# Performance work log

Hardware: AMD Instinct MI355X
Metric: run time of the kernel (lower is better)

## Reference

```python
import jax, jax.numpy as jnp
import numpy as np

B, C_IN, C_OUT, N, L = 4, 128, 256, 4096, 4
D = C_OUT // 4
EPS_BN = 1e-5


def setup_inputs() -> dict:
    key = jax.random.key(0)
    ks = jax.random.split(key, 16)
    s_in = 1.0 / np.sqrt(C_IN)
    s_out = 1.0 / np.sqrt(C_OUT)
    return {
        "features": jax.random.normal(ks[0], (B, C_IN, N), dtype=jnp.float32),
        # LBR: conv1x1 -> BN -> ReLU -> conv1x1 -> BN -> ReLU
        "lbr_w1": jax.random.uniform(ks[1], (C_OUT, C_IN), jnp.float32, -s_in, s_in),
        "lbr_g1": jnp.ones((C_OUT,), jnp.float32),
        "lbr_b1": jnp.zeros((C_OUT,), jnp.float32),
        "lbr_w2": jax.random.uniform(ks[2], (C_OUT, C_OUT), jnp.float32, -s_out, s_out),
        "lbr_g2": jnp.ones((C_OUT,), jnp.float32),
        "lbr_b2": jnp.zeros((C_OUT,), jnp.float32),
        # per-layer OffsetAttention params (stacked on leading L axis)
        # q_conv and k_conv share the same weight (q_conv.weight = k_conv.weight)
        "attn_qk_w": jax.random.uniform(ks[3], (L, D, C_OUT), jnp.float32, -s_out, s_out),
        "attn_v_w": jax.random.uniform(ks[4], (L, C_OUT, C_OUT), jnp.float32, -s_out, s_out),
        "attn_v_b": jax.random.uniform(ks[5], (L, C_OUT), jnp.float32, -s_out, s_out),
        "attn_t_w": jax.random.uniform(ks[6], (L, C_OUT, C_OUT), jnp.float32, -s_out, s_out),
        "attn_t_b": jax.random.uniform(ks[7], (L, C_OUT), jnp.float32, -s_out, s_out),
        "attn_bn_g": jnp.ones((L, C_OUT), jnp.float32),
        "attn_bn_b": jnp.zeros((L, C_OUT), jnp.float32),
    }


def batchnorm1d(x, gamma, beta):
    # x: [B, C, N]; training-mode BN: batch stats over (B, N), biased variance
    mean = jnp.mean(x, axis=(0, 2), keepdims=True)
    var = jnp.mean(jnp.square(x - mean), axis=(0, 2), keepdims=True)
    xn = (x - mean) * jax.lax.rsqrt(var + EPS_BN)
    return xn * gamma[None, :, None] + beta[None, :, None]


def offset_attention(x, qk_w, v_w, v_b, t_w, t_b, bn_g, bn_b):
    # x: [B, C, N]
    K = jnp.einsum("dc,bcn->bdn", qk_w, x)            # [B, D, N]
    # Q = same conv, permuted to [B, N, D]; attention_map = Q @ K -> [B, N, N]
    attn = jnp.einsum("bdn,bdm->bnm", K, K)
    attn = jax.nn.softmax(attn, axis=-1)
    # extra L1 renorm over dim=1 (column-wise)
    attn = attn / (1e-9 + jnp.sum(attn, axis=1, keepdims=True))
    V = jnp.einsum("dc,bcn->bdn", v_w, x) + v_b[None, :, None]  # [B, C, N]
    new_feat = jnp.einsum("bcn,bnm->bcm", V, attn)    # [B, C, N]
    off = x - new_feat
    t = jnp.einsum("dc,bcn->bdn", t_w, off) + t_b[None, :, None]
    return jax.nn.relu(batchnorm1d(t, bn_g, bn_b))


def reference(features, lbr_w1, lbr_g1, lbr_b1, lbr_w2, lbr_g2, lbr_b2,
              attn_qk_w, attn_v_w, attn_v_b, attn_t_w, attn_t_b,
              attn_bn_g, attn_bn_b):
    # LBR stem
    h = jnp.einsum("dc,bcn->bdn", lbr_w1, features)
    h = jax.nn.relu(batchnorm1d(h, lbr_g1, lbr_b1))
    h = jnp.einsum("dc,bcn->bdn", lbr_w2, h)
    h = jax.nn.relu(batchnorm1d(h, lbr_g2, lbr_b2))
    # stacked offset attention; output concatenates attention outputs only
    outs = []
    cur = h
    for i in range(L):
        cur = offset_attention(cur, attn_qk_w[i], attn_v_w[i], attn_v_b[i],
                               attn_t_w[i], attn_t_b[i], attn_bn_g[i], attn_bn_b[i])
        outs.append(cur)
    return jnp.concatenate(outs, axis=1)  # [B, C_OUT*L, N]
```

## Files before the change

### kernel.cpp

```cpp
#include <hip/hip_runtime.h>
#include <hip/hip_bf16.h>
#include <math.h>

#define NPTS 4096
#define CO   256
#define CI   128
#define BB   4
#define DQ   64
#define LL   4
#define PST  136

typedef __attribute__((ext_vector_type(8))) short bf16x8;
typedef __attribute__((ext_vector_type(4))) float f32x4;

#define MFMA16(a,b,c) __builtin_amdgcn_mfma_f32_16x16x32_bf16((a),(b),(c),0,0,0)

__device__ __forceinline__ short fb(float x) {
  __hip_bfloat16 h = __float2bfloat16(x);
  return __builtin_bit_cast(short, h);
}
__device__ __forceinline__ float bf(short s) {
  unsigned u = ((unsigned)(unsigned short)s) << 16;
  return __builtin_bit_cast(float, u);
}

__global__ __launch_bounds__(256) void cvtw_k(
    const float* __restrict__ S, short* __restrict__ D, int n8)
{
  const int i = blockIdx.x * 256 + threadIdx.x;
  if (i < n8) {
    const float4 a = ((const float4*)S)[i * 2];
    const float4 b = ((const float4*)S)[i * 2 + 1];
    bf16x8 r;
    r[0] = fb(a.x); r[1] = fb(a.y); r[2] = fb(a.z); r[3] = fb(a.w);
    r[4] = fb(b.x); r[5] = fb(b.y); r[6] = fb(b.z); r[7] = fb(b.w);
    ((bf16x8*)D)[i] = r;
  }
}

__global__ __launch_bounds__(256) void tcvt_k(
    const float* __restrict__ X, long xbs, int C, short* __restrict__ XT)
{
  const int n0 = blockIdx.x * 64, c0 = blockIdx.y * 64, b = blockIdx.z;
  const int t = threadIdx.x, tl = t & 63, tg = t >> 6;
  __shared__ float xs[64][65];
#pragma unroll
  for (int r = 0; r < 16; ++r) {
    const int cc = tg * 16 + r;
    xs[cc][tl] = X[(long)b * xbs + (long)(c0 + cc) * NPTS + n0 + tl];
  }
  __syncthreads();
#pragma unroll
  for (int r = 0; r < 16; ++r) {
    const int nn = tg * 16 + r;
    XT[((long)b * NPTS + n0 + nn) * C + c0 + tl] = fb(xs[tl][nn]);
  }
}

template<int OMODE, bool BIAS>
__global__ __launch_bounds__(256) void conv_a(
    const short* __restrict__ XT, int C,
    const short* __restrict__ Wb, const float* __restrict__ bias,
    void* __restrict__ Yv, long ybs)
{
  const int n0 = blockIdx.x * 128, d0 = blockIdx.y * 64, b = blockIdx.z;
  const int tid = threadIdx.x, w = tid >> 6, l = tid & 63, lg = l >> 4, lr = l & 15;
  const short* xb = XT + (long)b * NPTS * C;
  f32x4 acc[8];
#pragma unroll
  for (int i = 0; i < 8; ++i) acc[i] = (f32x4){0.f, 0.f, 0.f, 0.f};
  const int dr = d0 + w * 16 + lr;
  for (int kc = 0; kc < C; kc += 32) {
    const bf16x8 af = *(const bf16x8*)&Wb[(long)dr * C + kc + lg * 8];
#pragma unroll
    for (int ni = 0; ni < 8; ++ni) {
      const bf16x8 bx = *(const bf16x8*)&xb[(long)(n0 + ni * 16 + lr) * C + kc + lg * 8];
      acc[ni] = MFMA16(af, bx, acc[ni]);
    }
  }
  float bv[4] = {0.f, 0.f, 0.f, 0.f};
  if (BIAS) {
    const float4 b4 = *(const float4*)&bias[d0 + w * 16 + lg * 4];
    bv[0] = b4.x; bv[1] = b4.y; bv[2] = b4.z; bv[3] = b4.w;
  }
  const int db = d0 + w * 16 + lg * 4;
#pragma unroll
  for (int ni = 0; ni < 8; ++ni) {
    const int n = n0 + ni * 16 + lr;
#pragma unroll
    for (int j = 0; j < 4; ++j) {
      const float o = acc[ni][j] + bv[j];
      if constexpr (OMODE == 0) {
        ((float*)Yv)[(long)b * ybs + (long)(db + j) * NPTS + n] = o;
      } else {
        ((short*)Yv)[(long)b * ybs + ((long)(n0 >> 7) * CO + db + j) * 128 + (n & 127)] = fb(o);
      }
    }
  }
}

__global__ __launch_bounds__(256) void conv_b(
    const short* __restrict__ XT, const short* __restrict__ Wb,
    short* __restrict__ KTo)
{
  const int n0 = blockIdx.x * 64, b = blockIdx.y;
  const int tid = threadIdx.x, w = tid >> 6, l = tid & 63, lg = l >> 4, lr = l & 15;
  const short* xb = XT + (long)b * NPTS * CO;
  f32x4 acc[4];
#pragma unroll
  for (int i = 0; i < 4; ++i) acc[i] = (f32x4){0.f, 0.f, 0.f, 0.f};
  const long nr = n0 + w * 16 + lr;
  for (int kc = 0; kc < CO; kc += 32) {
    const bf16x8 af = *(const bf16x8*)&xb[nr * CO + kc + lg * 8];
#pragma unroll
    for (int di = 0; di < 4; ++di) {
      const bf16x8 wf = *(const bf16x8*)&Wb[(long)(di * 16 + lr) * CO + kc + lg * 8];
      acc[di] = MFMA16(af, wf, acc[di]);
    }
  }
  short* Ko = KTo + (long)b * NPTS * DQ;
  const int nb = n0 + w * 16 + lg * 4;
#pragma unroll
  for (int j = 0; j < 4; ++j) {
#pragma unroll
    for (int di = 0; di < 4; ++di)
      Ko[(long)(nb + j) * DQ + di * 16 + lr] = fb(acc[di][j]);
  }
}

__global__ __launch_bounds__(256) void bnstats_k(
    const float* __restrict__ X, long xbs,
    float* __restrict__ mean, float* __restrict__ rstd)
{
  const int c = blockIdx.x, t = threadIdx.x;
  float s = 0.f, s2 = 0.f;
  for (int b = 0; b < BB; ++b) {
    const float4* p = (const float4*)(X + (long)b * xbs + (long)c * NPTS);
    for (int n = t; n < NPTS / 4; n += 256) {
      const float4 v = p[n];
      s  += v.x + v.y + v.z + v.w;
      s2 += v.x * v.x + v.y * v.y + v.z * v.z + v.w * v.w;
    }
  }
#pragma unroll
  for (int o = 32; o > 0; o >>= 1) { s += __shfl_down(s, o); s2 += __shfl_down(s2, o); }
  __shared__ float a1[4], a2[4];
  if ((t & 63) == 0) { a1[t >> 6] = s; a2[t >> 6] = s2; }
  __syncthreads();
  if (t == 0) {
    const float S  = a1[0] + a1[1] + a1[2] + a1[3];
    const float S2 = a2[0] + a2[1] + a2[2] + a2[3];
    const float m  = S / (float)(BB * NPTS);
    const float v  = S2 / (float)(BB * NPTS) - m * m;
    mean[c] = m;
    rstd[c] = rsqrtf(v + 1e-5f);
  }
}

template<bool WF32, bool WBF>
__global__ __launch_bounds__(256) void bnrelu_t(
    const float* __restrict__ X, long xbs,
    const float* __restrict__ mean, const float* __restrict__ rstd,
    const float* __restrict__ g, const float* __restrict__ be,
    float* __restrict__ Yf, long ybs, short* __restrict__ XT)
{
  const int n0 = blockIdx.x * 64, c0 = blockIdx.y * 64, b = blockIdx.z;
  const int t = threadIdx.x, tl = t & 63, tg = t >> 6;
  __shared__ float xs[64][65];
#pragma unroll
  for (int r = 0; r < 16; ++r) {
    const int cc = tg * 16 + r, c = c0 + cc;
    float v = X[(long)b * xbs + (long)c * NPTS + n0 + tl];
    v = fmaxf((v - mean[c]) * rstd[c] * g[c] + be[c], 0.f);
    if (WF32) Yf[(long)b * ybs + (long)c * NPTS + n0 + tl] = v;
    xs[cc][tl] = v;
  }
  __syncthreads();
  if (WBF) {
#pragma unroll
    for (int r = 0; r < 16; ++r) {
      const int nn = tg * 16 + r;
      XT[((long)b * NPTS + n0 + nn) * CO + c0 + tl] = fb(xs[tl][nn]);
    }
  }
}

__global__ __launch_bounds__(256) void rowstats_mfma(
    const short* __restrict__ KT, float* __restrict__ pmax, float* __restrict__ psum)
{
  const int bid = blockIdx.x;
  const int b = (bid >> 1) & 3;
  const int idx = (bid >> 3) * 2 + (bid & 1);
  const int n0 = (idx & 63) * 64;
  const int chunk = idx >> 6;
  const int tid = threadIdx.x, w = tid >> 6, l = tid & 63, lg = l >> 4, lr = l & 15;
  const short* Kb = KT + (long)b * NPTS * DQ;
  const int nr = n0 + w * 16 + lr;
  const bf16x8 a0 = *(const bf16x8*)&Kb[(long)nr * DQ + lg * 8];
  const bf16x8 a1 = *(const bf16x8*)&Kb[(long)nr * DQ + 32 + lg * 8];

  float mx[4][4], sm[4][4];
#pragma unroll
  for (int p = 0; p < 4; ++p)
#pragma unroll
    for (int j = 0; j < 4; ++j) { mx[p][j] = -INFINITY; sm[p][j] = 0.f; }

  const int mc = chunk * (NPTS / 4);
  for (int m0 = mc; m0 < mc + NPTS / 4; m0 += 64) {
#pragma unroll
    for (int p = 0; p < 4; ++p) {
      const bf16x8 b0 = *(const bf16x8*)&Kb[(long)(m0 + p * 16 + lr) * DQ + lg * 8];
      const bf16x8 b1 = *(const bf16x8*)&Kb[(long)(m0 + p * 16 + lr) * DQ + 32 + lg * 8];
      f32x4 s = {0.f, 0.f, 0.f, 0.f};
      s = MFMA16(a0, b0, s);
      s = MFMA16(a1, b1, s);
#pragma unroll
      for (int j = 0; j < 4; ++j) {
        const float d = s[j] - mx[p][j];
        const float e = __expf(-fabsf(d));
        const bool gt = d > 0.f;
        sm[p][j] = gt ? fmaf(sm[p][j], e, 1.f) : (sm[p][j] + e);
        mx[p][j] = gt ? s[j] : mx[p][j];
      }
    }
  }
#pragma unroll
  for (int p = 1; p < 4; ++p)
#pragma unroll
    for (int j = 0; j < 4; ++j) {
      const float m2 = fmaxf(mx[0][j], mx[p][j]);
      sm[0][j] = sm[0][j] * __expf(mx[0][j] - m2) + sm[p][j] * __expf(mx[p][j] - m2);
      mx[0][j] = m2;
    }

  float mx0 = mx[0][0], mx1 = mx[0][1], mx2 = mx[0][2], mx3 = mx[0][3];
  float sm0 = sm[0][0], sm1 = sm[0][1], sm2 = sm[0][2], sm3 = sm[0][3];
#define MRG(MX, SM, OFF) { const float om_ = __shfl_xor(MX, OFF); \
  const float os_ = __shfl_xor(SM, OFF); \
  const float m2_ = fmaxf(MX, om_); \
  SM = SM * __expf(MX - m2_) + os_ * __expf(om_ - m2_); MX = m2_; }
#pragma unroll
  for (int off = 1; off < 16; off <<= 1) {
    MRG(mx0, sm0, off); MRG(mx1, sm1, off);
    MRG(mx2, sm2, off); MRG(mx3, sm3, off);
  }
  if (lr == 0) {
    const long base = ((long)chunk * BB + b) * NPTS + n0 + w * 16 + lg * 4;
    pmax[base + 0] = mx0; pmax[base + 1] = mx1; pmax[base + 2] = mx2; pmax[base + 3] = mx3;
    psum[base + 0] = sm0; psum[base + 1] = sm1; psum[base + 2] = sm2; psum[base + 3] = sm3;
  }
}

__global__ __launch_bounds__(256) void combine_k(
    const float* __restrict__ pmax, const float* __restrict__ psum,
    float* __restrict__ rmax, float* __restrict__ rinv)
{
  const long i = (long)blockIdx.x * 256 + threadIdx.x;
  const long st = (long)BB * NPTS;
  float m = pmax[i];
  m = fmaxf(m, pmax[st + i]); m = fmaxf(m, pmax[2 * st + i]); m = fmaxf(m, pmax[3 * st + i]);
  const float s = psum[i] * __expf(pmax[i] - m)
                + psum[st + i] * __expf(pmax[st + i] - m)
                + psum[2 * st + i] * __expf(pmax[2 * st + i] - m)
                + psum[3 * st + i] * __expf(pmax[3 * st + i] - m);
  rmax[i] = m;
  rinv[i] = 1.f / s;
}

__global__ __launch_bounds__(512) void pass2_mfma(
    const short* __restrict__ KT, const short* __restrict__ Vblk,
    const float* __restrict__ rmax, const float* __restrict__ rinv,
    short* __restrict__ XO)
{
  const int bid = blockIdx.x;
  const int b  = (bid >> 1) & 3;
  const int m0 = ((bid >> 3) * 2 + (bid & 1)) * 64;
  const int tid = threadIdx.x;
  const int w = tid >> 6, l = tid & 63, lg = l >> 4, lr = l & 15;
  const int NT = NPTS / 128;

  const short* Kb = KT + (long)b * NPTS * DQ;
  const short* Vb = Vblk + (long)b * CO * NPTS;
  const float* rmb = rmax + (long)b * NPTS;
  const float* rib = rinv + (long)b * NPTS;

  __shared__ short Ps[2][64][PST];
  __shared__ float cspart[8][64];
  __shared__ float csum[64];

  bf16x8 bK[4][2];
#pragma unroll
  for (int ms = 0; ms < 4; ++ms) {
    bK[ms][0] = *(const bf16x8*)&Kb[(long)(m0 + ms * 16 + lr) * DQ + lg * 8];
    bK[ms][1] = *(const bf16x8*)&Kb[(long)(m0 + ms * 16 + lr) * DQ + 32 + lg * 8];
  }

  f32x4 acc[4][2];
#pragma unroll
  for (int i = 0; i < 4; ++i) {
    acc[i][0] = (f32x4){0.f, 0.f, 0.f, 0.f};
    acc[i][1] = (f32x4){0.f, 0.f, 0.f, 0.f};
  }
  float cs[4] = {0.f, 0.f, 0.f, 0.f};
  const int c0 = w * 32;
  const int nb = w * 16;

  bf16x8 a0, a1;
  float4 rm4, ri4;

  auto sblk = [&](int dbuf) {
    f32x4 s[4];
#pragma unroll
    for (int ms = 0; ms < 4; ++ms) {
      s[ms] = (f32x4){0.f, 0.f, 0.f, 0.f};
      s[ms] = MFMA16(a0, bK[ms][0], s[ms]);
      s[ms] = MFMA16(a1, bK[ms][1], s[ms]);
    }
#pragma unroll
    for (int ms = 0; ms < 4; ++ms) {
      const float p0 = __expf(s[ms][0] - rm4.x) * ri4.x;
      const float p1 = __expf(s[ms][1] - rm4.y) * ri4.y;
      const float p2 = __expf(s[ms][2] - rm4.z) * ri4.z;
      const float p3 = __expf(s[ms][3] - rm4.w) * ri4.w;
      cs[ms] += p0 + p1 + p2 + p3;
      const unsigned u0 = ((unsigned)(unsigned short)fb(p1) << 16) | (unsigned short)fb(p0);
      const unsigned u1 = ((unsigned)(unsigned short)fb(p3) << 16) | (unsigned short)fb(p2);
      *(uint2*)&Ps[dbuf][ms * 16 + lr][nb + lg * 4] = make_uint2(u0, u1);
    }
  };

  a0  = *(const bf16x8*)&Kb[(long)(nb + lr) * DQ + lg * 8];
  a1  = *(const bf16x8*)&Kb[(long)(nb + lr) * DQ + 32 + lg * 8];
  rm4 = *(const float4*)&rmb[nb + lg * 4];
  ri4 = *(const float4*)&rib[nb + lg * 4];
  sblk(0);
  a0  = *(const bf16x8*)&Kb[(long)(128 + nb + lr) * DQ + lg * 8];
  a1  = *(const bf16x8*)&Kb[(long)(128 + nb + lr) * DQ + 32 + lg * 8];
  rm4 = *(const float4*)&rmb[128 + nb + lg * 4];
  ri4 = *(const float4*)&rib[128 + nb + lg * 4];

  for (int i = 0; i < NT; ++i) {
    const int n0 = i * 128;
    asm volatile("s_waitcnt lgkmcnt(0)" ::: "memory");
    __builtin_amdgcn_s_barrier();

    const short* vt = Vb + (long)(n0 >> 7) * CO * 128;
    bf16x8 vf[4][2];
#pragma unroll
    for (int kc = 0; kc < 4; ++kc) {
      vf[kc][0] = *(const bf16x8*)&vt[(long)(c0 + lr) * 128 + kc * 32 + lg * 8];
      vf[kc][1] = *(const bf16x8*)&vt[(long)(c0 + 16 + lr) * 128 + kc * 32 + lg * 8];
    }
    bf16x8 pa[4][4];
#pragma unroll
    for (int kc = 0; kc < 4; ++kc)
#pragma unroll
      for (int ms = 0; ms < 4; ++ms)
        pa[ms][kc] = *(const bf16x8*)&Ps[i & 1][ms * 16 + lr][kc * 32 + lg * 8];

    if (i + 1 < NT) {
      sblk((i + 1) & 1);
      if (i + 2 < NT) {
        a0  = *(const bf16x8*)&Kb[(long)((i + 2) * 128 + nb + lr) * DQ + lg * 8];
        a1  = *(const bf16x8*)&Kb[(long)((i + 2) * 128 + nb + lr) * DQ + 32 + lg * 8];
        rm4 = *(const float4*)&rmb[(i + 2) * 128 + nb + lg * 4];
        ri4 = *(const float4*)&rib[(i + 2) * 128 + nb + lg * 4];
      }
    }

#pragma unroll
    for (int kc = 0; kc < 4; ++kc)
#pragma unroll
      for (int ms = 0; ms < 4; ++ms) {
        acc[ms][0] = MFMA16(pa[ms][kc], vf[kc][0], acc[ms][0]);
        acc[ms][1] = MFMA16(pa[ms][kc], vf[kc][1], acc[ms][1]);
      }
  }

  __syncthreads();
#pragma unroll
  for (int ms = 0; ms < 4; ++ms) {
    float csv = cs[ms];
    csv += __shfl_xor(csv, 16); csv += __shfl_xor(csv, 32);
    if (lg == 0) cspart[w][ms * 16 + lr] = csv;
  }
  __syncthreads();
  if (tid < 64) {
    float s = 0.f;
#pragma unroll
    for (int ww = 0; ww < 8; ++ww) s += cspart[ww][tid];
    csum[tid] = s;
  }
  __syncthreads();

  short* XOb = XO + (long)b * NPTS * CO;
#pragma unroll
  for (int ms = 0; ms < 4; ++ms) {
#pragma unroll
    for (int j = 0; j < 4; ++j) {
      const int m = m0 + ms * 16 + lg * 4 + j;
      const float inv = 1.f / (1e-9f + csum[ms * 16 + lg * 4 + j]);
      const long i0 = (long)m * CO + c0 + lr;
      const long i1 = (long)m * CO + c0 + 16 + lr;
      XOb[i0] = fb(bf(XOb[i0]) - acc[ms][0][j] * inv);
      XOb[i1] = fb(bf(XOb[i1]) - acc[ms][1][j] * inv);
    }
  }
}

extern "C" void kernel_launch(void* const* d_in, const int* in_sizes, int n_in,
                              void* d_out, int out_size, void* d_ws, size_t ws_size,
                              hipStream_t stream)
{
  const float* feat = (const float*)d_in[0];
  const float* w1   = (const float*)d_in[1];
  const float* g1   = (const float*)d_in[2];
  const float* b1   = (const float*)d_in[3];
  const float* w2   = (const float*)d_in[4];
  const float* g2   = (const float*)d_in[5];
  const float* b2   = (const float*)d_in[6];
  const float* qkw  = (const float*)d_in[7];
  const float* vw   = (const float*)d_in[8];
  const float* vb   = (const float*)d_in[9];
  const float* tw   = (const float*)d_in[10];
  const float* tb   = (const float*)d_in[11];
  const float* bng  = (const float*)d_in[12];
  const float* bnb  = (const float*)d_in[13];

  float* out = (float*)d_out;

  short* xt    = (short*)d_ws;
  short* KTb   = xt + (long)BB * NPTS * CO;
  short* Vblk  = KTb + (long)BB * NPTS * DQ;
  short* wb1   = Vblk + (long)BB * CO * NPTS;
  short* wb2   = wb1 + (long)CO * CI;
  short* wqk   = wb2 + (long)CO * CO;
  short* wv    = wqk + (long)LL * DQ * CO;
  short* wt    = wv + (long)LL * CO * CO;
  float* pmaxb = (float*)(wt + (long)LL * CO * CO);
  float* psumb = pmaxb + (long)4 * BB * NPTS;
  float* rmaxb = psumb + (long)4 * BB * NPTS;
  float* rinvb = rmaxb + (long)BB * NPTS;
  float* meanb = rinvb + (long)BB * NPTS;
  float* rstdb = meanb + CO;

  const long OBS = (long)LL * CO * NPTS;
  float* h1 = out + (long)2 * CO * NPTS;
  float* x0 = out + (long)1 * CO * NPTS;

  const dim3 blk(256);

  cvtw_k<<<dim3((CO * CI / 8 + 255) / 256), blk, 0, stream>>>(w1, wb1, CO * CI / 8);
  cvtw_k<<<dim3((CO * CO / 8 + 255) / 256), blk, 0, stream>>>(w2, wb2, CO * CO / 8);
  cvtw_k<<<dim3((LL * DQ * CO / 8 + 255) / 256), blk, 0, stream>>>(qkw, wqk, LL * DQ * CO / 8);
  cvtw_k<<<dim3((LL * CO * CO / 8 + 255) / 256), blk, 0, stream>>>(vw, wv, LL * CO * CO / 8);
  cvtw_k<<<dim3((LL * CO * CO / 8 + 255) / 256), blk, 0, stream>>>(tw, wt, LL * CO * CO / 8);

  tcvt_k<<<dim3(64, 2, BB), blk, 0, stream>>>(feat, (long)CI * NPTS, CI, xt);
  conv_a<0, false><<<dim3(32, 4, BB), blk, 0, stream>>>(xt, CI, wb1, nullptr, h1, OBS);
  bnstats_k<<<dim3(CO), blk, 0, stream>>>(h1, OBS, meanb, rstdb);
  bnrelu_t<false, true><<<dim3(64, 4, BB), blk, 0, stream>>>(
      h1, OBS, meanb, rstdb, g1, b1, nullptr, 0, xt);
  conv_a<0, false><<<dim3(32, 4, BB), blk, 0, stream>>>(xt, CO, wb2, nullptr, x0, OBS);
  bnstats_k<<<dim3(CO), blk, 0, stream>>>(x0, OBS, meanb, rstdb);
  bnrelu_t<false, true><<<dim3(64, 4, BB), blk, 0, stream>>>(
      x0, OBS, meanb, rstdb, g2, b2, nullptr, 0, xt);

  for (int lyr = 0; lyr < LL; ++lyr) {
    float* nft = out + (long)lyr * CO * NPTS;
    conv_b<<<dim3(64, BB), blk, 0, stream>>>(xt, wqk + (long)lyr * DQ * CO, KTb);
    conv_a<1, true><<<dim3(32, 4, BB), blk, 0, stream>>>(
        xt, CO, wv + (long)lyr * CO * CO, vb + (long)lyr * CO, Vblk, (long)CO * NPTS);
    rowstats_mfma<<<dim3(1024), blk, 0, stream>>>(KTb, pmaxb, psumb);
    combine_k<<<dim3(BB * NPTS / 256), blk, 0, stream>>>(pmaxb, psumb, rmaxb, rinvb);
    pass2_mfma<<<dim3(256), dim3(512), 0, stream>>>(KTb, Vblk, rmaxb, rinvb, xt);
    conv_a<0, true><<<dim3(32, 4, BB), blk, 0, stream>>>(
        xt, CO, wt + (long)lyr * CO * CO, tb + (long)lyr * CO, nft, OBS);
    bnstats_k<<<dim3(CO), blk, 0, stream>>>(nft, OBS, meanb, rstdb);
    if (lyr < LL - 1) {
      bnrelu_t<true, true><<<dim3(64, 4, BB), blk, 0, stream>>>(
          nft, OBS, meanb, rstdb, bng + (long)lyr * CO, bnb + (long)lyr * CO, nft, OBS, xt);
    } else {
      bnrelu_t<true, false><<<dim3(64, 4, BB), blk, 0, stream>>>(
          nft, OBS, meanb, rstdb, bng + (long)lyr * CO, bnb + (long)lyr * CO, nft, OBS, nullptr);
    }
  }
}
```

Measured before the change: 949.3 us.

## Widen pass2 attention kernel to 1024 threads with 256-wide key tiles

The fused attention-times-V kernel now uses 16 waves per block instead of 8. Each wave computes 16 output channels rather than 32, and each iteration processes a 256-key tile instead of 128. The software pipeline, where the next tile's scores were computed while the current P tile was consumed, is replaced by a simpler loop: compute P, barrier, then run the MFMAs, with P fragments read from LDS inline. This halves per-wave accumulator and register pressure and the number of barriers, but gives up the overlap between score computation and the PV matmul and doubles LDS use for P.

```diff
diff --git a/kernel.cpp b/kernel.cpp
--- a/kernel.cpp
+++ b/kernel.cpp
@@ -8,7 +8,7 @@
 #define BB   4
 #define DQ   64
 #define LL   4
-#define PST  136
+#define PST2 264
 
 typedef __attribute__((ext_vector_type(8))) short bf16x8;
 typedef __attribute__((ext_vector_type(4))) float f32x4;
@@ -267,7 +267,7 @@
   rinv[i] = 1.f / s;
 }
 
-__global__ __launch_bounds__(512) void pass2_mfma(
+__global__ __launch_bounds__(1024) void pass2_mfma(
     const short* __restrict__ KT, const short* __restrict__ Vblk,
     const float* __restrict__ rmax, const float* __restrict__ rinv,
     short* __restrict__ XO)
@@ -277,15 +277,15 @@
   const int m0 = ((bid >> 3) * 2 + (bid & 1)) * 64;
   const int tid = threadIdx.x;
   const int w = tid >> 6, l = tid & 63, lg = l >> 4, lr = l & 15;
-  const int NT = NPTS / 128;
+  const int NT = NPTS / 256;
 
   const short* Kb = KT + (long)b * NPTS * DQ;
   const short* Vb = Vblk + (long)b * CO * NPTS;
   const float* rmb = rmax + (long)b * NPTS;
   const float* rib = rinv + (long)b * NPTS;
 
-  __shared__ short Ps[2][64][PST];
-  __shared__ float cspart[8][64];
+  __shared__ short Ps[2][64][PST2];
+  __shared__ float cspart[16][64];
   __shared__ float csum[64];
 
   bf16x8 bK[4][2];
@@ -295,20 +295,26 @@
     bK[ms][1] = *(const bf16x8*)&Kb[(long)(m0 + ms * 16 + lr) * DQ + 32 + lg * 8];
   }
 
-  f32x4 acc[4][2];
-#pragma unroll
-  for (int i = 0; i < 4; ++i) {
-    acc[i][0] = (f32x4){0.f, 0.f, 0.f, 0.f};
-    acc[i][1] = (f32x4){0.f, 0.f, 0.f, 0.f};
-  }
+  f32x4 acc[4];
+#pragma unroll
+  for (int i = 0; i < 4; ++i) acc[i] = (f32x4){0.f, 0.f, 0.f, 0.f};
   float cs[4] = {0.f, 0.f, 0.f, 0.f};
-  const int c0 = w * 32;
+  const int c0 = w * 16;
   const int nb = w * 16;
 
-  bf16x8 a0, a1;
-  float4 rm4, ri4;
-
-  auto sblk = [&](int dbuf) {
+  bf16x8 a0 = *(const bf16x8*)&Kb[(long)(nb + lr) * DQ + lg * 8];
+  bf16x8 a1 = *(const bf16x8*)&Kb[(long)(nb + lr) * DQ + 32 + lg * 8];
+  float4 rm4 = *(const float4*)&rmb[nb + lg * 4];
+  float4 ri4 = *(const float4*)&rib[nb + lg * 4];
+
+  for (int i = 0; i < NT; ++i) {
+    const int n0 = i * 256;
+    bf16x8 vf[8];
+#pragma unroll
+    for (int kc = 0; kc < 8; ++kc) {
+      const short* vt = Vb + (long)((n0 >> 7) + (kc >> 2)) * CO * 128;
+      vf[kc] = *(const bf16x8*)&vt[(long)(c0 + lr) * 128 + (kc & 3) * 32 + lg * 8];
+    }
     f32x4 s[4];
 #pragma unroll
     for (int ms = 0; ms < 4; ++ms) {
@@ -325,56 +331,26 @@
       cs[ms] += p0 + p1 + p2 + p3;
       const unsigned u0 = ((unsigned)(unsigned short)fb(p1) << 16) | (unsigned short)fb(p0);
       const unsigned u1 = ((unsigned)(unsigned short)fb(p3) << 16) | (unsigned short)fb(p2);
-      *(uint2*)&Ps[dbuf][ms * 16 + lr][nb + lg * 4] = make_uint2(u0, u1);
-    }
-  };
-
-  a0  = *(const bf16x8*)&Kb[(long)(nb + lr) * DQ + lg * 8];
-  a1  = *(const bf16x8*)&Kb[(long)(nb + lr) * DQ + 32 + lg * 8];
-  rm4 = *(const float4*)&rmb[nb + lg * 4];
-  ri4 = *(const float4*)&rib[nb + lg * 4];
-  sblk(0);
-  a0  = *(const bf16x8*)&Kb[(long)(128 + nb + lr) * DQ + lg * 8];
-  a1  = *(const bf16x8*)&Kb[(long)(128 + nb + lr) * DQ + 32 + lg * 8];
-  rm4 = *(const float4*)&rmb[128 + nb + lg * 4];
-  ri4 = *(const float4*)&rib[128 + nb + lg * 4];
-
-  for (int i = 0; i < NT; ++i) {
-    const int n0 = i * 128;
+      *(uint2*)&Ps[i & 1][ms * 16 + lr][nb + lg * 4] = make_uint2(u0, u1);
+    }
+    if (i + 1 < NT) {
+      const int nn = (i + 1) * 256 + nb;
+      a0  = *(const bf16x8*)&Kb[(long)(nn + lr) * DQ + lg * 8];
+      a1  = *(const bf16x8*)&Kb[(long)(nn + lr) * DQ + 32 + lg * 8];
+      rm4 = *(const float4*)&rmb[nn + lg * 4];
+      ri4 = *(const float4*)&rib[nn + lg * 4];
+    }
     asm volatile("s_waitcnt lgkmcnt(0)" ::: "memory");
     __builtin_amdgcn_s_barrier();
-
-    const short* vt = Vb + (long)(n0 >> 7) * CO * 128;
-    bf16x8 vf[4][2];
-#pragma unroll
-    for (int kc = 0; kc < 4; ++kc) {
-      vf[kc][0] = *(const bf16x8*)&vt[(long)(c0 + lr) * 128 + kc * 32 + lg * 8];
-      vf[kc][1] = *(const bf16x8*)&vt[(long)(c0 + 16 + lr) * 128 + kc * 32 + lg * 8];
-    }
-    bf16x8 pa[4][4];
-#pragma unroll
-    for (int kc = 0; kc < 4; ++kc)
-#pragma unroll
-      for (int ms = 0; ms < 4; ++ms)
-        pa[ms][kc] = *(const bf16x8*)&Ps[i & 1][ms * 16 + lr][kc * 32 + lg * 8];
-
-    if (i + 1 < NT) {
-      sblk((i + 1) & 1);
-      if (i + 2 < NT) {
-        a0  = *(const bf16x8*)&Kb[(long)((i + 2) * 128 + nb + lr) * DQ + lg * 8];
-        a1  = *(const bf16x8*)&Kb[(long)((i + 2) * 128 + nb + lr) * DQ + 32 + lg * 8];
-        rm4 = *(const float4*)&rmb[(i + 2) * 128 + nb + lg * 4];
-        ri4 = *(const float4*)&rib[(i + 2) * 128 + nb + lg * 4];
+    asm volatile("" ::: "memory");
+#pragma unroll
+    for (int kc = 0; kc < 8; ++kc) {
+#pragma unroll
+      for (int ms = 0; ms < 4; ++ms) {
+        const bf16x8 pa = *(const bf16x8*)&Ps[i & 1][ms * 16 + lr][kc * 32 + lg * 8];
+        acc[ms] = MFMA16(pa, vf[kc], acc[ms]);
       }
     }
-
-#pragma unroll
-    for (int kc = 0; kc < 4; ++kc)
-#pragma unroll
-      for (int ms = 0; ms < 4; ++ms) {
-        acc[ms][0] = MFMA16(pa[ms][kc], vf[kc][0], acc[ms][0]);
-        acc[ms][1] = MFMA16(pa[ms][kc], vf[kc][1], acc[ms][1]);
-      }
   }
 
   __syncthreads();
@@ -388,7 +364,7 @@
   if (tid < 64) {
     float s = 0.f;
 #pragma unroll
-    for (int ww = 0; ww < 8; ++ww) s += cspart[ww][tid];
+    for (int ww = 0; ww < 16; ++ww) s += cspart[ww][tid];
     csum[tid] = s;
   }
   __syncthreads();
@@ -401,9 +377,7 @@
       const int m = m0 + ms * 16 + lg * 4 + j;
       const float inv = 1.f / (1e-9f + csum[ms * 16 + lg * 4 + j]);
       const long i0 = (long)m * CO + c0 + lr;
-      const long i1 = (long)m * CO + c0 + 16 + lr;
-      XOb[i0] = fb(bf(XOb[i0]) - acc[ms][0][j] * inv);
-      XOb[i1] = fb(bf(XOb[i1]) - acc[ms][1][j] * inv);
+      XOb[i0] = fb(bf(XOb[i0]) - acc[ms][j] * inv);
     }
   }
 }
@@ -473,7 +447,7 @@
         xt, CO, wv + (long)lyr * CO * CO, vb + (long)lyr * CO, Vblk, (long)CO * NPTS);
     rowstats_mfma<<<dim3(1024), blk, 0, stream>>>(KTb, pmaxb, psumb);
     combine_k<<<dim3(BB * NPTS / 256), blk, 0, stream>>>(pmaxb, psumb, rmaxb, rinvb);
-    pass2_mfma<<<dim3(256), dim3(512), 0, stream>>>(KTb, Vblk, rmaxb, rinvb, xt);
+    pass2_mfma<<<dim3(256), dim3(1024), 0, stream>>>(KTb, Vblk, rmaxb, rinvb, xt);
     conv_a<0, true><<<dim3(32, 4, BB), blk, 0, stream>>>(
         xt, CO, wt + (long)lyr * CO * CO, tb + (long)lyr * CO, nft, OBS);
     bnstats_k<<<dim3(CO), blk, 0, stream>>>(nft, OBS, meanb, rstdb);
```

Result: slower. 1.057 ms (+11.3%).
